# Kernel optimization log

Hardware: AMD Instinct MI355X
Metric: run time of the kernel (lower is better)

The kernel has to match this reference:

```python
import jax, jax.numpy as jnp
import numpy as np

BATCH = 10000
NUM_TREES = 1000
NUM_NODES = 511  # full binary tree of depth 8
N_FEATURES = 256
N_CLASSES = 1
MAX_DEPTH = 8


def setup_inputs() -> dict:
    key = jax.random.key(0)
    k = jax.random.split(key, 6)
    flat = NUM_TREES * NUM_NODES
    x = jax.random.normal(k[0], (BATCH, N_FEATURES), dtype=jnp.float32)
    thresholds = jax.random.normal(k[1], (flat,), dtype=jnp.float32)
    values = jax.random.normal(k[2], (flat, N_CLASSES), dtype=jnp.float32)
    lefts = jax.random.randint(k[3], (flat,), 0, NUM_NODES).astype(jnp.int64)
    rights = jax.random.randint(k[4], (flat,), 0, NUM_NODES).astype(jnp.int64)
    features = jax.random.randint(k[5], (flat,), 0, N_FEATURES).astype(jnp.int64)
    return {
        "x": x,
        "thresholds": thresholds,
        "values": values,
        "lefts": lefts,
        "rights": rights,
        "features": features,
        "num_trees": NUM_TREES,
        "num_nodes": NUM_NODES,
        "max_depth": MAX_DEPTH,
    }


def reference(x, thresholds, values, lefts, rights, features, num_trees, num_nodes, max_depth):
    batch = x.shape[0]
    # nodes_offset: flat index of each tree's root in the concatenated node arrays
    nodes_offset = (jnp.arange(num_trees, dtype=jnp.int32) * num_nodes)[None, :]  # [1, T]
    indexes = jnp.broadcast_to(nodes_offset, (batch, num_trees))  # [B, T]
    for _ in range(max_depth):
        feature_nodes = features[indexes]                     # [B, T] feature id per current node
        feature_values = jnp.take_along_axis(x, feature_nodes, axis=1)  # [B, T]
        thr = thresholds[indexes]                             # [B, T]
        l = lefts[indexes]                                    # [B, T]
        r = rights[indexes]                                   # [B, T]
        indexes = jnp.where(feature_values >= thr, r, l) + nodes_offset
    output = values[indexes]  # [B, T, C]
    return output
```

## Files before the change

kernel.cpp:

```cpp
#include <hip/hip_runtime.h>
#include <stdint.h>

#define BATCH     10000
#define NUM_TREES 1000
#define NUM_NODES 511
#define NFEAT     256
#define DEPTH     8
#define FLAT_NODES (NUM_TREES * NUM_NODES)

#define TREE_BYTES 1360
#define VLEAF_OFF  ((size_t)NUM_TREES * TREE_BYTES)
#define WS_NEEDED  (VLEAF_OFF + (size_t)NUM_TREES * 256 * 4)

#define BT 64
#define TT 64
#define NTHREADS 1024
#define XS_BYTES  (NFEAT * 64 * 4)
#define OUT_LD    36
#define OS_BYTES  (64 * OUT_LD * 4)
#define SH_BYTES  (XS_BYTES + OS_BYTES)

__global__ __launch_bounds__(256)
void unroll_kernel(const float* __restrict__ thr,
                   const int* __restrict__ feats,
                   const int* __restrict__ lefts,
                   const int* __restrict__ rights,
                   const float* __restrict__ values,
                   unsigned char* __restrict__ ws) {
  __shared__ uint16_t n_s[4][512];
  const int wv = threadIdx.x >> 6, lane = threadIdx.x & 63;
  const int tree = blockIdx.x * 4 + wv;
  const int base = tree * NUM_NODES;
  uint16_t* n = n_s[wv];
  uint4* rec   = (uint4*)(ws + (size_t)tree * TREE_BYTES);
  float* vleaf = (float*)(ws + VLEAF_OFF + (size_t)tree * 1024);

  if (lane == 0) n[0] = 0;
  __syncthreads();
  const int EBASE[4] = {0, 1, 5, 21};
  #pragma unroll
  for (int d = 0; d < 8; ++d) {
    const int lvl = (1 << d) - 1, cnt = 1 << d;
    for (int i = lane; i < cnt; i += 64) {
      int p  = lvl + i;
      int np = n[p];
      int nl = lefts[base + np], nr = rights[base + np];
      n[2 * p + 1] = (uint16_t)nl;
      n[2 * p + 2] = (uint16_t)nr;
      if ((d & 1) == 0) {
        uint32_t f3 = (uint32_t)feats[base + np] |
                      ((uint32_t)feats[base + nl] << 8) |
                      ((uint32_t)feats[base + nr] << 16);
        rec[EBASE[d >> 1] + i] =
            make_uint4(__float_as_uint(thr[base + np]),
                       __float_as_uint(thr[base + nl]),
                       __float_as_uint(thr[base + nr]), f3);
      }
    }
    __syncthreads();
  }
  #pragma unroll
  for (int i = lane; i < 256; i += 64)
    vleaf[i] = values[base + n[255 + i]];
}

__global__ __launch_bounds__(NTHREADS, 8)
void traverse64(const float* __restrict__ x,
                const unsigned char* __restrict__ ws,
                float* __restrict__ out) {
  extern __shared__ unsigned char smem[];
  float* x_s   = (float*)smem;
  float* out_s = (float*)(smem + XS_BYTES);

  const int tid  = threadIdx.x;
  const int wid  = tid >> 6;
  const int lane = tid & 63;
  const int b0   = blockIdx.y * BT;
  const int t0   = blockIdx.x * TT;

  {
    const float4* xg = (const float4*)x;
    #pragma unroll
    for (int p = 0; p < 4; ++p) {
      int i = tid + p * NTHREADS;
      int r = i >> 6, c = i & 63;
      int gb = b0 + r;
      float4 v = (gb < BATCH) ? xg[(size_t)gb * 64 + c]
                              : make_float4(0.f, 0.f, 0.f, 0.f);
      int o = (c << 8) + (r ^ (c & 31));
      x_s[o]       = v.x;
      x_s[o + 64]  = v.y;
      x_s[o + 128] = v.z;
      x_s[o + 192] = v.w;
    }
  }
  __syncthreads();

  const unsigned char* nb = ws + (size_t)(t0 + 4 * wid) * TREE_BYTES;
  int loc[4] = {0, 0, 0, 0};
  #pragma unroll
  for (int it = 0; it < 4; ++it) {
    const int eoff = (it == 0) ? 0 : (it == 1) ? 16 : (it == 2) ? 80 : 336;
    uint4 r[4];
    #pragma unroll
    for (int c = 0; c < 4; ++c)
      r[c] = *(const uint4*)(nb + (size_t)c * TREE_BYTES + loc[c] * 16 + eoff);
    float xp[4];
    #pragma unroll
    for (int c = 0; c < 4; ++c) {
      int fp = r[c].w & 255;
      xp[c] = x_s[(fp << 6) + (lane ^ ((fp >> 2) & 31))];
    }
    bool  c0[4]; int fc[4]; float tc[4];
    #pragma unroll
    for (int c = 0; c < 4; ++c) {
      c0[c] = (xp[c] >= __uint_as_float(r[c].x));
      fc[c] = c0[c] ? ((r[c].w >> 16) & 255) : ((r[c].w >> 8) & 255);
      tc[c] = __uint_as_float(c0[c] ? r[c].z : r[c].y);
    }
    float xc[4];
    #pragma unroll
    for (int c = 0; c < 4; ++c)
      xc[c] = x_s[(fc[c] << 6) + (lane ^ ((fc[c] >> 2) & 31))];
    #pragma unroll
    for (int c = 0; c < 4; ++c)
      loc[c] = 4 * loc[c] + 2 * (int)c0[c] + (int)(xc[c] >= tc[c]);
  }
  const float* vl = (const float*)(ws + VLEAF_OFF);
  float4 v;
  {
    const int gt0 = t0 + 4 * wid;
    int g0 = (gt0 + 0 < NUM_TREES) ? gt0 + 0 : 0;
    int g1 = (gt0 + 1 < NUM_TREES) ? gt0 + 1 : 0;
    int g2 = (gt0 + 2 < NUM_TREES) ? gt0 + 2 : 0;
    int g3 = (gt0 + 3 < NUM_TREES) ? gt0 + 3 : 0;
    v = make_float4(vl[(size_t)g0 * 256 + loc[0]],
                    vl[(size_t)g1 * 256 + loc[1]],
                    vl[(size_t)g2 * 256 + loc[2]],
                    vl[(size_t)g3 * 256 + loc[3]]);
  }

  if (wid < 8)
    *(float4*)(out_s + lane * OUT_LD + 4 * wid) = v;
  __syncthreads();
  {
    int col = tid & 31, rr = tid >> 5;
    #pragma unroll
    for (int k = 0; k < 2; ++k) {
      int row = rr + 32 * k;
      int gb = b0 + row, gt = t0 + col;
      if (gb < BATCH && gt < NUM_TREES)
        out[(size_t)gb * NUM_TREES + gt] = out_s[row * OUT_LD + col];
    }
  }
  __syncthreads();
  if (wid >= 8)
    *(float4*)(out_s + lane * OUT_LD + 4 * (wid - 8)) = v;
  __syncthreads();
  {
    int col = tid & 31, rr = tid >> 5;
    #pragma unroll
    for (int k = 0; k < 2; ++k) {
      int row = rr + 32 * k;
      int gb = b0 + row, gt = t0 + 32 + col;
      if (gb < BATCH && gt < NUM_TREES)
        out[(size_t)gb * NUM_TREES + gt] = out_s[row * OUT_LD + col];
    }
  }
}

#define FB_BT 64
#define FB_TT 64
#define FB_TPR 16
#define FB_NROUNDS 4
#define FB_NTHREADS 1024
#define FB_XS (NFEAT * 64 * 4)
#define FB_NSU (FB_TPR * NUM_NODES)
#define FB_NS (FB_NSU * 8)
#define FB_OLD (FB_TT + 1)
#define FB_OS (FB_BT * FB_OLD * 4)
#define FB_SH (FB_XS + FB_NS + FB_OS)
#define FB_PREF ((FB_NSU + FB_NTHREADS - 1) / FB_NTHREADS)

__global__ __launch_bounds__(FB_NTHREADS, 1)
void fb_traverse(const float* __restrict__ x,
                 const float* __restrict__ thrg,
                 const int* __restrict__ featg,
                 const int* __restrict__ leftg,
                 const int* __restrict__ rightg,
                 const float* __restrict__ values,
                 float* __restrict__ out) {
  extern __shared__ unsigned char smem[];
  float* x_s     = (float*)smem;
  uint2* nodes_s = (uint2*)(smem + FB_XS);
  float* out_s   = (float*)(smem + FB_XS + FB_NS);
  const int tid = threadIdx.x, wid = tid >> 6, lane = tid & 63;
  const int b0 = blockIdx.y * FB_BT, t0 = blockIdx.x * FB_TT;
  uint2 pf[FB_PREF];
  auto load_round = [&](int rr) {
    const int gbase = (t0 + rr * FB_TPR) * NUM_NODES;
    #pragma unroll
    for (int k = 0; k < FB_PREF; ++k) {
      int fi = tid + k * FB_NTHREADS;
      uint2 v = make_uint2(0u, 0u);
      if (fi < FB_NSU) {
        int gi = gbase + fi;
        if (gi < FLAT_NODES) {
          uint32_t meta = (uint32_t)featg[gi] | ((uint32_t)leftg[gi] << 8) |
                          ((uint32_t)rightg[gi] << 20);
          v = make_uint2(__float_as_uint(thrg[gi]), meta);
        }
      }
      pf[k] = v;
    }
  };
  auto write_nodes = [&]() {
    #pragma unroll
    for (int k = 0; k < FB_PREF; ++k) {
      int fi = tid + k * FB_NTHREADS;
      if (fi < FB_NSU) nodes_s[fi] = pf[k];
    }
  };
  load_round(0);
  {
    const float4* xg = (const float4*)x;
    #pragma unroll
    for (int p = 0; p < (FB_BT * (NFEAT / 4)) / FB_NTHREADS; ++p) {
      int i = tid + p * FB_NTHREADS;
      int r = i >> 6, c = i & 63;
      int gb = b0 + r;
      float4 v = make_float4(0.f, 0.f, 0.f, 0.f);
      if (gb < BATCH) v = xg[gb * (NFEAT / 4) + c];
      int o = (c << 8) + (r ^ (c & 31));
      x_s[o] = v.x; x_s[o + 64] = v.y; x_s[o + 128] = v.z; x_s[o + 192] = v.w;
    }
  }
  write_nodes();
  __syncthreads();
  for (int r = 0; r < FB_NROUNDS; ++r) {
    if (r + 1 < FB_NROUNDS) load_round(r + 1);
    const uint2* nA = nodes_s + wid * NUM_NODES;
    const int tr0 = t0 + r * FB_TPR;
    const int gta = tr0 + wid;
    const int offA = (gta < NUM_TREES ? gta : 0) * NUM_NODES;
    uint2 na = nA[0];
    float va = 0.f;
    #pragma unroll
    for (int d = 0; d < DEPTH; ++d) {
      int fa = na.y & 0xFF;
      int la = (na.y >> 8) & 0xFFF;
      int ra = (int)(na.y >> 20);
      float xa = x_s[(fa << 6) + (lane ^ ((fa >> 2) & 31))];
      if (d < DEPTH - 1) {
        uint2 nla = nA[la], nra = nA[ra];
        na = (xa >= __uint_as_float(na.x)) ? nra : nla;
      } else {
        float vla = values[offA + la], vra = values[offA + ra];
        va = (xa >= __uint_as_float(na.x)) ? vra : vla;
      }
    }
    out_s[lane * FB_OLD + r * FB_TPR + wid] = va;
    __syncthreads();
    if (r + 1 < FB_NROUNDS) { write_nodes(); __syncthreads(); }
  }
  {
    const int gt = t0 + lane;
    #pragma unroll
    for (int p = 0; p < FB_BT / 16; ++p) {
      int rr = p * 16 + wid;
      int gb = b0 + rr;
      if (gb < BATCH && gt < NUM_TREES)
        out[gb * NUM_TREES + gt] = out_s[rr * FB_OLD + lane];
    }
  }
}

extern "C" void kernel_launch(void* const* d_in, const int* in_sizes, int n_in,
                              void* d_out, int out_size, void* d_ws, size_t ws_size,
                              hipStream_t stream) {
  const float* x          = (const float*)d_in[0];
  const float* thresholds = (const float*)d_in[1];
  const float* values     = (const float*)d_in[2];
  const int*   lefts      = (const int*)d_in[3];
  const int*   rights     = (const int*)d_in[4];
  const int*   features   = (const int*)d_in[5];
  float* out = (float*)d_out;

  if (ws_size >= WS_NEEDED) {
    unsigned char* ws = (unsigned char*)d_ws;
    unroll_kernel<<<NUM_TREES / 4, 256, 0, stream>>>(
        thresholds, features, lefts, rights, values, ws);
    hipFuncSetAttribute(reinterpret_cast<const void*>(traverse64),
                        hipFuncAttributeMaxDynamicSharedMemorySize, SH_BYTES);
    dim3 grid((NUM_TREES + TT - 1) / TT, (BATCH + BT - 1) / BT);
    traverse64<<<grid, NTHREADS, SH_BYTES, stream>>>(x, ws, out);
  } else {
    hipFuncSetAttribute(reinterpret_cast<const void*>(fb_traverse),
                        hipFuncAttributeMaxDynamicSharedMemorySize, FB_SH);
    dim3 grid((NUM_TREES + FB_TT - 1) / FB_TT, (BATCH + FB_BT - 1) / FB_BT);
    fb_traverse<<<grid, FB_NTHREADS, FB_SH, stream>>>(
        x, thresholds, features, lefts, rights, values, out);
  }
}
```

Baseline: 55.64 us.

## Pre-transpose x in workspace and load tiles via direct global-to-LDS copies

Adds a transpose kernel that writes x as a feature-major padded array in the workspace. The traversal kernel then fills its shared x tile with global_load_lds 16-byte copies instead of register-staged scattered stores. It also drops the XOR swizzle on the gather index. The cost is an extra kernel launch and a full read and write of x, about 10 MB each way. Whether this path runs depends on the workspace being large enough, and dropping the swizzle may bring back LDS bank conflicts.

```diff
diff --git a/kernel.cpp b/kernel.cpp
--- a/kernel.cpp
+++ b/kernel.cpp
@@ -11,6 +11,10 @@
 #define TREE_BYTES 1360
 #define VLEAF_OFF  ((size_t)NUM_TREES * TREE_BYTES)
 #define WS_NEEDED  (VLEAF_OFF + (size_t)NUM_TREES * 256 * 4)
+#define XT_LD      10048
+#define XT_OFF     WS_NEEDED
+#define XT_BYTES   ((size_t)NFEAT * XT_LD * 4)
+#define WS_XT      (XT_OFF + XT_BYTES)
 
 #define BT 64
 #define TT 64
@@ -19,6 +23,12 @@
 #define OUT_LD    36
 #define OS_BYTES  (64 * OUT_LD * 4)
 #define SH_BYTES  (XS_BYTES + OS_BYTES)
+
+__device__ __forceinline__ void glds16(const void* g, void* l) {
+  __builtin_amdgcn_global_load_lds(
+      (const __attribute__((address_space(1))) unsigned int*)g,
+      (__attribute__((address_space(3))) unsigned int*)l, 16, 0, 0);
+}
 
 __global__ __launch_bounds__(256)
 void unroll_kernel(const float* __restrict__ thr,
@@ -64,6 +74,36 @@
     vleaf[i] = values[base + n[255 + i]];
 }
 
+__global__ __launch_bounds__(256)
+void transpose_kernel(const float* __restrict__ x, float* __restrict__ xT) {
+  __shared__ float tile[64][65];
+  const int tid = threadIdx.x;
+  const int b0 = blockIdx.x * 64, f0 = blockIdx.y * 64;
+  const float4* xg = (const float4*)x;
+  #pragma unroll
+  for (int p = 0; p < 4; ++p) {
+    int i = tid + p * 256;
+    int r = i >> 4, c4 = i & 15;
+    int gb = b0 + r;
+    float4 v = (gb < BATCH) ? xg[(size_t)gb * 64 + (f0 >> 2) + c4]
+                            : make_float4(0.f, 0.f, 0.f, 0.f);
+    tile[r][4 * c4 + 0] = v.x;
+    tile[r][4 * c4 + 1] = v.y;
+    tile[r][4 * c4 + 2] = v.z;
+    tile[r][4 * c4 + 3] = v.w;
+  }
+  __syncthreads();
+  #pragma unroll
+  for (int p = 0; p < 4; ++p) {
+    int i = tid + p * 256;
+    int fr = i >> 4, b4 = i & 15;
+    float4 w = make_float4(tile[4 * b4 + 0][fr], tile[4 * b4 + 1][fr],
+                           tile[4 * b4 + 2][fr], tile[4 * b4 + 3][fr]);
+    *(float4*)(xT + (size_t)(f0 + fr) * XT_LD + b0 + 4 * b4) = w;
+  }
+}
+
+template <bool XT>
 __global__ __launch_bounds__(NTHREADS, 8)
 void traverse64(const float* __restrict__ x,
                 const unsigned char* __restrict__ ws,
@@ -78,7 +118,16 @@
   const int b0   = blockIdx.y * BT;
   const int t0   = blockIdx.x * TT;
 
-  {
+  if (XT) {
+    const float* xT = (const float*)(ws + XT_OFF);
+    #pragma unroll
+    for (int k = 0; k < 4; ++k) {
+      int fi = tid + k * NTHREADS;
+      int f = fi >> 4, c16 = fi & 15;
+      glds16(xT + (size_t)f * XT_LD + b0 + 4 * c16,
+             (unsigned char*)x_s + (size_t)fi * 16);
+    }
+  } else {
     const float4* xg = (const float4*)x;
     #pragma unroll
     for (int p = 0; p < 4; ++p) {
@@ -96,6 +145,11 @@
   }
   __syncthreads();
 
+  auto xgather = [&](int f) -> float {
+    if (XT) return x_s[(f << 6) + lane];
+    return x_s[(f << 6) + (lane ^ ((f >> 2) & 31))];
+  };
+
   const unsigned char* nb = ws + (size_t)(t0 + 4 * wid) * TREE_BYTES;
   int loc[4] = {0, 0, 0, 0};
   #pragma unroll
@@ -107,10 +161,8 @@
       r[c] = *(const uint4*)(nb + (size_t)c * TREE_BYTES + loc[c] * 16 + eoff);
     float xp[4];
     #pragma unroll
-    for (int c = 0; c < 4; ++c) {
-      int fp = r[c].w & 255;
-      xp[c] = x_s[(fp << 6) + (lane ^ ((fp >> 2) & 31))];
-    }
+    for (int c = 0; c < 4; ++c)
+      xp[c] = xgather(r[c].w & 255);
     bool  c0[4]; int fc[4]; float tc[4];
     #pragma unroll
     for (int c = 0; c < 4; ++c) {
@@ -121,7 +173,7 @@
     float xc[4];
     #pragma unroll
     for (int c = 0; c < 4; ++c)
-      xc[c] = x_s[(fc[c] << 6) + (lane ^ ((fc[c] >> 2) & 31))];
+      xc[c] = xgather(fc[c]);
     #pragma unroll
     for (int c = 0; c < 4; ++c)
       loc[c] = 4 * loc[c] + 2 * (int)c0[c] + (int)(xc[c] >= tc[c]);
@@ -286,14 +338,24 @@
   const int*   features   = (const int*)d_in[5];
   float* out = (float*)d_out;
 
-  if (ws_size >= WS_NEEDED) {
+  if (ws_size >= WS_XT) {
     unsigned char* ws = (unsigned char*)d_ws;
     unroll_kernel<<<NUM_TREES / 4, 256, 0, stream>>>(
         thresholds, features, lefts, rights, values, ws);
-    hipFuncSetAttribute(reinterpret_cast<const void*>(traverse64),
+    transpose_kernel<<<dim3((BATCH + 63) / 64, NFEAT / 64), 256, 0, stream>>>(
+        x, (float*)(ws + XT_OFF));
+    hipFuncSetAttribute(reinterpret_cast<const void*>(traverse64<true>),
                         hipFuncAttributeMaxDynamicSharedMemorySize, SH_BYTES);
     dim3 grid((NUM_TREES + TT - 1) / TT, (BATCH + BT - 1) / BT);
-    traverse64<<<grid, NTHREADS, SH_BYTES, stream>>>(x, ws, out);
+    traverse64<true><<<grid, NTHREADS, SH_BYTES, stream>>>(x, ws, out);
+  } else if (ws_size >= WS_NEEDED) {
+    unsigned char* ws = (unsigned char*)d_ws;
+    unroll_kernel<<<NUM_TREES / 4, 256, 0, stream>>>(
+        thresholds, features, lefts, rights, values, ws);
+    hipFuncSetAttribute(reinterpret_cast<const void*>(traverse64<false>),
+                        hipFuncAttributeMaxDynamicSharedMemorySize, SH_BYTES);
+    dim3 grid((NUM_TREES + TT - 1) / TT, (BATCH + BT - 1) / BT);
+    traverse64<false><<<grid, NTHREADS, SH_BYTES, stream>>>(x, ws, out);
   } else {
     hipFuncSetAttribute(reinterpret_cast<const void*>(fb_traverse),
                         hipFuncAttributeMaxDynamicSharedMemorySize, FB_SH);
```

Result: slower. 57.97 us (+4.2%).
